# Performance work log

Measured on AMD Instinct MI355X. Metric: run time of the kernel, lower is better.

## Reference

```python
import jax, jax.numpy as jnp
import numpy as np

N = 50000      # nodes
E = 800000     # directed edges (self-loops added in reference)
F_IN = 64      # input features
HID = 64       # hidden channels
HEADS = 4
NCLS = 3
G = 64         # graphs in batch
EPS = 1e-5
NEG_SLOPE = 0.2


def setup_inputs() -> dict:
    key = jax.random.key(0)
    ks = jax.random.split(key, 20)
    s = 0.1
    inp = {
        "x": jax.random.normal(ks[0], (N, F_IN), jnp.float32),
        "edge_index": jax.random.randint(ks[1], (2, E), 0, N, jnp.int64),
        "batch": jnp.sort(jax.random.randint(ks[2], (N,), 0, G, jnp.int64)),
        # GATConv 1: F_IN -> HID per head, HEADS heads, concat
        "W1": jax.random.normal(ks[3], (F_IN, HEADS * HID), jnp.float32) * s,
        "a_src1": jax.random.normal(ks[4], (HEADS, HID), jnp.float32) * s,
        "a_dst1": jax.random.normal(ks[5], (HEADS, HID), jnp.float32) * s,
        "b1": jnp.zeros((HEADS * HID,), jnp.float32),
        # BatchNorm1d(256) eval-mode params
        "g1": jnp.ones((HEADS * HID,), jnp.float32),
        "be1": jnp.zeros((HEADS * HID,), jnp.float32),
        "m1": jnp.zeros((HEADS * HID,), jnp.float32),
        "v1": jnp.ones((HEADS * HID,), jnp.float32),
        # GATConv 2: 256 -> HID, 1 head
        "W2": jax.random.normal(ks[6], (HEADS * HID, HID), jnp.float32) * s,
        "a_src2": jax.random.normal(ks[7], (1, HID), jnp.float32) * s,
        "a_dst2": jax.random.normal(ks[8], (1, HID), jnp.float32) * s,
        "b2": jnp.zeros((HID,), jnp.float32),
        # BatchNorm1d(64)
        "g2": jnp.ones((HID,), jnp.float32),
        "be2": jnp.zeros((HID,), jnp.float32),
        "m2": jnp.zeros((HID,), jnp.float32),
        "v2": jnp.ones((HID,), jnp.float32),
        # MLP head
        "lw1": jax.random.normal(ks[9], (HID, HID // 2), jnp.float32) * s,
        "lb1": jnp.zeros((HID // 2,), jnp.float32),
        "lw2": jax.random.normal(ks[10], (HID // 2, NCLS), jnp.float32) * s,
        "lb2": jnp.zeros((NCLS,), jnp.float32),
    }
    return inp


def _gat(x, src, dst, W, a_s, a_d, b):
    """PyG-style GATConv: gather, LeakyReLU score, segment-softmax over dst, scatter-add."""
    H_, C_ = a_s.shape
    h = (x @ W).reshape(-1, H_, C_)                       # [N,H,C]
    es = jnp.einsum('nhc,hc->nh', h, a_s)                 # per-node src score
    ed = jnp.einsum('nhc,hc->nh', h, a_d)                 # per-node dst score
    e = jax.nn.leaky_relu(es[src] + ed[dst], NEG_SLOPE)   # [Etot,H]
    m = jax.ops.segment_max(e, dst, num_segments=N)       # stable softmax per dst
    p = jnp.exp(e - m[dst])
    denom = jax.ops.segment_sum(p, dst, num_segments=N)
    alpha = p / denom[dst]                                # [Etot,H]
    out = jax.ops.segment_sum(h[src] * alpha[:, :, None], dst, num_segments=N)
    return out.reshape(-1, H_ * C_) + b


def _bn(x, g, b, mean, var):
    return (x - mean) * jax.lax.rsqrt(var + EPS) * g + b


def reference(x, W1, a_src1, a_dst1, b1, g1, be1, m1, v1,
              W2, a_src2, a_dst2, b2, g2, be2, m2, v2,
              lw1, lb1, lw2, lb2, edge_index, batch):
    loop = jnp.arange(N, dtype=edge_index.dtype)
    src = jnp.concatenate([edge_index[0], loop])          # add self-loops
    dst = jnp.concatenate([edge_index[1], loop])
    h = _gat(x, src, dst, W1, a_src1, a_dst1, b1)
    h = jax.nn.elu(_bn(h, g1, be1, m1, v1))
    h = _gat(h, src, dst, W2, a_src2, a_dst2, b2)
    h = _bn(h, g2, be2, m2, v2)
    # global_mean_pool over graphs
    sums = jax.ops.segment_sum(h, batch, num_segments=G)
    cnt = jax.ops.segment_sum(jnp.ones((N, 1), h.dtype), batch, num_segments=G)
    pooled = sums / jnp.maximum(cnt, 1.0)                 # [G, HID]
    z = jax.nn.relu(pooled @ lw1 + lb1)
    z = z @ lw2 + lb2
    return jax.nn.log_softmax(z, axis=1)
```

## Files before the change

### kernel.cpp

```cpp
#include <hip/hip_runtime.h>
#include <math.h>

#define N_NODES 50000
#define N_EDGES 800000
#define ETOT    (N_EDGES + N_NODES)
#define GGRAPHS 64
#define EPS_BN  1e-5f

typedef __attribute__((ext_vector_type(8))) short short8;
typedef __attribute__((ext_vector_type(4))) float f32x4;
typedef __attribute__((ext_vector_type(2))) float f32x2;

__device__ __forceinline__ unsigned short f2bf(float f) {
    union { float f; unsigned u; } v; v.f = f;
    unsigned r = v.u + 0x7fffu + ((v.u >> 16) & 1u);
    return (unsigned short)(r >> 16);
}
__device__ __forceinline__ float leaky(float e) {
    return fmaxf(e, 0.2f * e);
}
__device__ __forceinline__ unsigned pack4_fp8(float a, float b, float c, float d) {
    int v = __builtin_amdgcn_cvt_pk_fp8_f32(a, b, 0, false);
    v = __builtin_amdgcn_cvt_pk_fp8_f32(c, d, v, true);
    return (unsigned)v;
}
__device__ __forceinline__ short8 cvt8(const float* p) {
    float4 u = *(const float4*)p;
    float4 v = *(const float4*)(p + 4);
    short8 r;
    r[0] = (short)f2bf(u.x); r[1] = (short)f2bf(u.y);
    r[2] = (short)f2bf(u.z); r[3] = (short)f2bf(u.w);
    r[4] = (short)f2bf(v.x); r[5] = (short)f2bf(v.y);
    r[6] = (short)f2bf(v.z); r[7] = (short)f2bf(v.w);
    return r;
}

#define NBUK 196
#define EPB  4096
#define NBLK2 ((ETOT + EPB - 1) / EPB)
#define CAP  8192


#define PREP2_T (32768 + 320)

__global__ void k_prep(const float* __restrict__ W1, const float* __restrict__ W2,
                       const float* __restrict__ b1, const float* __restrict__ g1,
                       const float* __restrict__ be1, const float* __restrict__ m1,
                       const float* __restrict__ v1,
                       const float* __restrict__ b2, const float* __restrict__ g2,
                       const float* __restrict__ be2, const float* __restrict__ m2,
                       const float* __restrict__ v2,
                       unsigned short* __restrict__ W1T,
                       unsigned short* __restrict__ W2T,
                       float* __restrict__ A1s, float* __restrict__ B1s,
                       float* __restrict__ A2s, float* __restrict__ B2s) {
    int t = blockIdx.x * 256 + threadIdx.x;
    if (t < 16384) {
        int i = t;
        int n = i >> 6, k = i & 63;
        W1T[i] = f2bf(W1[k * 256 + n]);
    } else if (t < 32768) {
        int i = t - 16384;
        int n = i >> 8, kp = i & 255;
        int rk = (kp & 15) * 16 + (kp >> 4);
        W2T[i] = f2bf(W2[rk * 64 + n]);
    } else if (t < 32768 + 256) {
        int z = t - 32768;
        int r = (z & 15) * 16 + (z >> 4);
        float A = g1[r] * rsqrtf(v1[r] + EPS_BN);
        A1s[z] = A;
        B1s[z] = (b1[r] - m1[r]) * A + be1[r];
    } else if (t < PREP2_T) {
        int z = t - 32768 - 256;
        int r = (z & 3) * 16 + (z >> 2);
        float A = g2[r] * rsqrtf(v2[r] + EPS_BN);
        A2s[z] = A;
        B2s[z] = (b2[r] - m2[r]) * A + be2[r];
    }
}


__global__ __launch_bounds__(256)
void k_bhist(const int* __restrict__ ei, int* __restrict__ gcnt) {
    __shared__ int c[NBUK];
    int t = threadIdx.x;
    for (int i = t; i < NBUK; i += 256) c[i] = 0;
    __syncthreads();
    int e0 = blockIdx.x * EPB;
#pragma unroll
    for (int j = 0; j < EPB / 256; ++j) {
        int e = e0 + j * 256 + t;
        if (e < ETOT) {
            int d = (e < N_EDGES) ? ei[N_EDGES + e] : (e - N_EDGES);
            atomicAdd(&c[d >> 8], 1);
        }
    }
    __syncthreads();
    for (int i = t; i < NBUK; i += 256) gcnt[i * NBLK2 + blockIdx.x] = c[i];
}

__global__ __launch_bounds__(256)
void k_bsum(const int* __restrict__ gcnt, int* __restrict__ bstart,
            int* __restrict__ offs) {
    __shared__ int s[256];
    int t = threadIdx.x;
    int total = 0;
    if (t < NBUK)
        for (int b = 0; b < NBLK2; ++b) total += gcnt[t * NBLK2 + b];
    s[t] = total; __syncthreads();
    for (int d2 = 1; d2 < 256; d2 <<= 1) {
        int add = (t >= d2) ? s[t - d2] : 0;
        __syncthreads();
        s[t] += add;
        __syncthreads();
    }
    if (t < NBUK) bstart[t] = s[t] - total;
    if (t == 0) { bstart[NBUK] = ETOT; offs[N_NODES] = ETOT; }
}

__global__ __launch_bounds__(256)
void k_bscan(const int* __restrict__ gcnt, const int* __restrict__ bstart,
             int* __restrict__ gbase) {
    __shared__ int s[256];
    int b = blockIdx.x, t = threadIdx.x;
    int v = (t < NBLK2) ? gcnt[b * NBLK2 + t] : 0;
    s[t] = v; __syncthreads();
    for (int d2 = 1; d2 < 256; d2 <<= 1) {
        int add = (t >= d2) ? s[t - d2] : 0;
        __syncthreads();
        s[t] += add;
        __syncthreads();
    }
    int base = bstart[b];
    if (t < NBLK2) gbase[b * NBLK2 + t] = base + s[t] - v;
}

__global__ __launch_bounds__(256)
void k_bfill(const int* __restrict__ ei, const int* __restrict__ gbase,
             unsigned* __restrict__ pairs) {
    __shared__ int cur[NBUK];
    int t = threadIdx.x;
    for (int i = t; i < NBUK; i += 256) cur[i] = gbase[i * NBLK2 + blockIdx.x];
    __syncthreads();
    int e0 = blockIdx.x * EPB;
#pragma unroll
    for (int j = 0; j < EPB / 256; ++j) {
        int e = e0 + j * 256 + t;
        if (e < ETOT) {
            int s, d;
            if (e < N_EDGES) { s = ei[e]; d = ei[N_EDGES + e]; }
            else             { s = d = e - N_EDGES; }
            int pos = atomicAdd(&cur[d >> 8], 1);
            pairs[pos] = (unsigned)s | ((unsigned)d << 16);
        }
    }
}

__global__ __launch_bounds__(256)
void k_csr(const unsigned* __restrict__ pairs, const int* __restrict__ bstart,
           int* __restrict__ offs, unsigned short* __restrict__ csr) {
    __shared__ unsigned sp[CAP];
    __shared__ unsigned short lc[CAP];
    __shared__ int c256[256];
    __shared__ int o256[256];
    __shared__ int s[256];
    int b = blockIdx.x, t = threadIdx.x;
    int base = bstart[b];
    int n = bstart[b + 1] - base;
    int node = b * 256 + t;
    if (n <= CAP) {
        for (int i = t; i < n; i += 256) sp[i] = pairs[base + i];
        c256[t] = 0;
        __syncthreads();
        for (int i = t; i < n; i += 256) atomicAdd(&c256[(sp[i] >> 16) & 255], 1);
        __syncthreads();
        int v = c256[t];
        s[t] = v; __syncthreads();
        for (int d2 = 1; d2 < 256; d2 <<= 1) {
            int add = (t >= d2) ? s[t - d2] : 0;
            __syncthreads();
            s[t] += add;
            __syncthreads();
        }
        int myoff = s[t] - v;
        o256[t] = myoff;
        if (node < N_NODES) offs[node] = base + myoff;
        __syncthreads();
        for (int i = t; i < n; i += 256) {
            unsigned p = sp[i];
            int pos = atomicAdd(&o256[(p >> 16) & 255], 1);
            lc[pos] = (unsigned short)(p & 0xffff);
        }
        __syncthreads();
        for (int i = t; i < n; i += 256) csr[base + i] = lc[i];
    } else {
        c256[t] = 0;
        __syncthreads();
        for (int i = t; i < n; i += 256) atomicAdd(&c256[(pairs[base + i] >> 16) & 255], 1);
        __syncthreads();
        int v = c256[t];
        s[t] = v; __syncthreads();
        for (int d2 = 1; d2 < 256; d2 <<= 1) {
            int add = (t >= d2) ? s[t - d2] : 0;
            __syncthreads();
            s[t] += add;
            __syncthreads();
        }
        int myoff = s[t] - v;
        o256[t] = base + myoff;
        if (node < N_NODES) offs[node] = base + myoff;
        __syncthreads();
        for (int i = t; i < n; i += 256) {
            unsigned p = pairs[base + i];
            int pos = atomicAdd(&o256[(p >> 16) & 255], 1);
            csr[pos] = (unsigned short)(p & 0xffff);
        }
    }
}


__global__ __launch_bounds__(256)
void k_gemm1(const float* __restrict__ x, const unsigned short* __restrict__ W1Tg,
             const float* __restrict__ a_s, const float* __restrict__ a_d,
             unsigned char* __restrict__ h1f8, float* __restrict__ es1, float* __restrict__ ed1) {
    __shared__ unsigned short W1T[256 * 72];
    int t = threadIdx.x;
    for (int c = t; c < 2048; c += 256) {
        int n = c >> 3, k8 = (c & 7) * 8;
        *(short8*)&W1T[n * 72 + k8] = *(const short8*)&W1Tg[n * 64 + k8];
    }
    __syncthreads();
    int wid = t >> 6, lane = t & 63;
    int quad = lane >> 4, col = lane & 15;
    float as_r[16], ad_r[16];
#pragma unroll
    for (int i = 0; i < 16; ++i) {
        as_r[i] = a_s[i * 16 + col];
        ad_r[i] = a_d[i * 16 + col];
    }
    int tile = blockIdx.x * 4 + wid;
    if (tile >= 3125) return;
    int base = tile * 16;
    short8 a0 = cvt8(&x[(size_t)(base + col) * 64 + quad * 8]);
    short8 a1 = cvt8(&x[(size_t)(base + col) * 64 + 32 + quad * 8]);
    f32x4 acc[16];
#pragma unroll
    for (int nt = 0; nt < 16; ++nt) acc[nt] = (f32x4){0.f, 0.f, 0.f, 0.f};
#pragma unroll
    for (int nt = 0; nt < 16; ++nt) {
        short8 b0 = *(const short8*)&W1T[(nt * 16 + col) * 72 + quad * 8];
        short8 b1 = *(const short8*)&W1T[(nt * 16 + col) * 72 + 32 + quad * 8];
        acc[nt] = __builtin_amdgcn_mfma_f32_16x16x32_bf16(a0, b0, acc[nt], 0, 0, 0);
        acc[nt] = __builtin_amdgcn_mfma_f32_16x16x32_bf16(a1, b1, acc[nt], 0, 0, 0);
    }
    float esp[16], edp[16];
#pragma unroll
    for (int i = 0; i < 16; ++i) { esp[i] = 0.f; edp[i] = 0.f; }
#pragma unroll
    for (int nt = 0; nt < 16; ++nt) {
        int hd = nt >> 2;
#pragma unroll
        for (int r = 0; r < 4; ++r) {
            esp[hd * 4 + r] += acc[nt][r] * as_r[nt];
            edp[hd * 4 + r] += acc[nt][r] * ad_r[nt];
        }
    }
#pragma unroll
    for (int i = 0; i < 16; ++i) {
        float v = esp[i], w = edp[i];
#pragma unroll
        for (int m = 1; m <= 8; m <<= 1) { v += __shfl_xor(v, m); w += __shfl_xor(w, m); }
        esp[i] = v; edp[i] = w;
    }
    if (col == 0) {
#pragma unroll
        for (int hd = 0; hd < 4; ++hd)
#pragma unroll
            for (int r = 0; r < 4; ++r) {
                int node = base + quad * 4 + r;
                es1[node * 4 + hd] = esp[hd * 4 + r];
                ed1[node * 4 + hd] = edp[hd * 4 + r];
            }
    }
#pragma unroll
    for (int r = 0; r < 4; ++r) {
        uint4 pk;
        pk.x = pack4_fp8(acc[0][r],  acc[1][r],  acc[2][r],  acc[3][r]);
        pk.y = pack4_fp8(acc[4][r],  acc[5][r],  acc[6][r],  acc[7][r]);
        pk.z = pack4_fp8(acc[8][r],  acc[9][r],  acc[10][r], acc[11][r]);
        pk.w = pack4_fp8(acc[12][r], acc[13][r], acc[14][r], acc[15][r]);
        *(uint4*)&h1f8[(size_t)(base + quad * 4 + r) * 256 + col * 16] = pk;
    }
}


__global__ __launch_bounds__(256)
void k_gat1(const unsigned char* __restrict__ h1f8, const float* __restrict__ es1,
            const float* __restrict__ ed1, const int* __restrict__ offs,
            const unsigned short* __restrict__ csr,
            const float* __restrict__ A1s, const float* __restrict__ B1s,
            unsigned short* __restrict__ hb) {
    int tid = threadIdx.x;
    int l = tid & 63;
    int gbase = l & 48;
    int q = tid & 15;
    int d = blockIdx.x * 16 + (tid >> 4);
    int start = offs[d], deg = offs[d + 1] - start;
    int e4 = q >> 2, hd = q & 3;
    float edv = ed1[d * 4 + hd];
    const unsigned char* hrow = h1f8 + q * 16;
    float a[16];
#pragma unroll
    for (int i = 0; i < 16; ++i) a[i] = 0.f;
    float wsum = 0.f;
    for (int c0 = 0; c0 < deg; c0 += 4) {
        int idx = c0 + e4;
        int s = csr[start + min(idx, deg - 1)];
        float w = (idx < deg) ? __expf(leaky(es1[s * 4 + hd] + edv)) : 0.f;
        wsum += w;
        int se[4];
#pragma unroll
        for (int e = 0; e < 4; ++e) se[e] = __shfl(s, gbase | (e << 2));
        uint4 rv[4];
#pragma unroll
        for (int e = 0; e < 4; ++e)
            rv[e] = *(const uint4*)(hrow + ((size_t)(unsigned)se[e] << 8));
#pragma unroll
        for (int e = 0; e < 4; ++e) {
            float w0 = __shfl(w, gbase | (e << 2) | 0);
            float w1 = __shfl(w, gbase | (e << 2) | 1);
            float w2 = __shfl(w, gbase | (e << 2) | 2);
            float w3 = __shfl(w, gbase | (e << 2) | 3);
            f32x2 p;
            p = __builtin_amdgcn_cvt_pk_f32_fp8((int)rv[e].x, false); a[0]  += w0 * p.x; a[1]  += w0 * p.y;
            p = __builtin_amdgcn_cvt_pk_f32_fp8((int)rv[e].x, true);  a[2]  += w0 * p.x; a[3]  += w0 * p.y;
            p = __builtin_amdgcn_cvt_pk_f32_fp8((int)rv[e].y, false); a[4]  += w1 * p.x; a[5]  += w1 * p.y;
            p = __builtin_amdgcn_cvt_pk_f32_fp8((int)rv[e].y, true);  a[6]  += w1 * p.x; a[7]  += w1 * p.y;
            p = __builtin_amdgcn_cvt_pk_f32_fp8((int)rv[e].z, false); a[8]  += w2 * p.x; a[9]  += w2 * p.y;
            p = __builtin_amdgcn_cvt_pk_f32_fp8((int)rv[e].z, true);  a[10] += w2 * p.x; a[11] += w2 * p.y;
            p = __builtin_amdgcn_cvt_pk_f32_fp8((int)rv[e].w, false); a[12] += w3 * p.x; a[13] += w3 * p.y;
            p = __builtin_amdgcn_cvt_pk_f32_fp8((int)rv[e].w, true);  a[14] += w3 * p.x; a[15] += w3 * p.y;
        }
    }
    wsum += __shfl_xor(wsum, 4);
    wsum += __shfl_xor(wsum, 8);
    float inv[4];
#pragma unroll
    for (int h = 0; h < 4; ++h) inv[h] = 1.f / __shfl(wsum, gbase | h);
    ushort4 ov[4];
#pragma unroll
    for (int i0 = 0; i0 < 4; ++i0) {
        float4 Av = *(const float4*)&A1s[q * 16 + i0 * 4];
        float4 Bv = *(const float4*)&B1s[q * 16 + i0 * 4];
        float o0 = a[i0 * 4 + 0] * inv[i0] * Av.x + Bv.x;
        float o1 = a[i0 * 4 + 1] * inv[i0] * Av.y + Bv.y;
        float o2 = a[i0 * 4 + 2] * inv[i0] * Av.z + Bv.z;
        float o3 = a[i0 * 4 + 3] * inv[i0] * Av.w + Bv.w;
        o0 = (o0 > 0.f) ? o0 : expm1f(o0);
        o1 = (o1 > 0.f) ? o1 : expm1f(o1);
        o2 = (o2 > 0.f) ? o2 : expm1f(o2);
        o3 = (o3 > 0.f) ? o3 : expm1f(o3);
        ov[i0].x = f2bf(o0); ov[i0].y = f2bf(o1); ov[i0].z = f2bf(o2); ov[i0].w = f2bf(o3);
    }
#pragma unroll
    for (int i0 = 0; i0 < 4; ++i0)
        *(ushort4*)&hb[(size_t)d * 256 + q * 16 + i0 * 4] = ov[i0];
}


__global__ __launch_bounds__(256)
void k_gemm2(const unsigned short* __restrict__ hbbf, const unsigned short* __restrict__ W2Tg,
             const float* __restrict__ a_s, const float* __restrict__ a_d,
             unsigned char* __restrict__ h2f8, float* __restrict__ es2, float* __restrict__ ed2) {
    __shared__ unsigned short W2T[64 * 264];
    int t = threadIdx.x;
    for (int c = t; c < 2048; c += 256) {
        int n = c >> 5, k8 = (c & 31) * 8;
        *(short8*)&W2T[n * 264 + k8] = *(const short8*)&W2Tg[n * 256 + k8];
    }
    __syncthreads();
    int wid = t >> 6, lane = t & 63;
    int quad = lane >> 4, col = lane & 15;
    float as_r[4], ad_r[4];
#pragma unroll
    for (int i = 0; i < 4; ++i) {
        as_r[i] = a_s[i * 16 + col];
        ad_r[i] = a_d[i * 16 + col];
    }
    int tile = blockIdx.x * 4 + wid;
    if (tile >= 3125) return;
    int base = tile * 16;
    short8 af[8];
#pragma unroll
    for (int kk = 0; kk < 8; ++kk)
        af[kk] = *(const short8*)&hbbf[(size_t)(base + col) * 256 + kk * 32 + quad * 8];
    f32x4 acc[4];
#pragma unroll
    for (int nt = 0; nt < 4; ++nt) acc[nt] = (f32x4){0.f, 0.f, 0.f, 0.f};
#pragma unroll
    for (int kk = 0; kk < 8; ++kk) {
#pragma unroll
        for (int nt = 0; nt < 4; ++nt) {
            short8 b = *(const short8*)&W2T[(nt * 16 + col) * 264 + kk * 32 + quad * 8];
            acc[nt] = __builtin_amdgcn_mfma_f32_16x16x32_bf16(af[kk], b, acc[nt], 0, 0, 0);
        }
    }
    float esp[4], edp[4];
#pragma unroll
    for (int r = 0; r < 4; ++r) { esp[r] = 0.f; edp[r] = 0.f; }
#pragma unroll
    for (int nt = 0; nt < 4; ++nt)
#pragma unroll
        for (int r = 0; r < 4; ++r) {
            esp[r] += acc[nt][r] * as_r[nt];
            edp[r] += acc[nt][r] * ad_r[nt];
        }
#pragma unroll
    for (int r = 0; r < 4; ++r) {
        float v = esp[r], w = edp[r];
#pragma unroll
        for (int m = 1; m <= 8; m <<= 1) { v += __shfl_xor(v, m); w += __shfl_xor(w, m); }
        esp[r] = v; edp[r] = w;
    }
    if (col == 0) {
#pragma unroll
        for (int r = 0; r < 4; ++r) {
            int node = base + quad * 4 + r;
            es2[node] = esp[r];
            ed2[node] = edp[r];
        }
    }
#pragma unroll
    for (int r = 0; r < 4; ++r) {
        unsigned pk = pack4_fp8(acc[0][r], acc[1][r], acc[2][r], acc[3][r]);
        *(unsigned*)&h2f8[(size_t)(base + quad * 4 + r) * 64 + col * 4] = pk;
    }
}


__global__ __launch_bounds__(256)
void k_gat2(const unsigned char* __restrict__ h2f8, const float* __restrict__ es2,
            const float* __restrict__ ed2, const int* __restrict__ offs,
            const unsigned short* __restrict__ csr,
            const float* __restrict__ A2s, const float* __restrict__ B2s,
            float* __restrict__ out2) {
    int tid = threadIdx.x;
    int l = tid & 63;
    int gbase = l & 48;
    int q = tid & 15;
    int d = blockIdx.x * 16 + (tid >> 4);
    int start = offs[d], deg = offs[d + 1] - start;
    float edv = ed2[d];
    const unsigned char* hrow = h2f8 + q * 4;
    float a0 = 0.f, a1 = 0.f, a2 = 0.f, a3 = 0.f, wsum = 0.f;
    int e4 = q & 3;
    for (int c0 = 0; c0 < deg; c0 += 4) {
        int idx = c0 + e4;
        int s = csr[start + min(idx, deg - 1)];
        float w = (idx < deg) ? __expf(leaky(es2[s] + edv)) : 0.f;
        wsum += w;
        int se[4];
#pragma unroll
        for (int e = 0; e < 4; ++e) se[e] = __shfl(s, gbase | e);
        unsigned rv[4];
#pragma unroll
        for (int e = 0; e < 4; ++e)
            rv[e] = *(const unsigned*)(hrow + ((size_t)(unsigned)se[e] << 6));
#pragma unroll
        for (int e = 0; e < 4; ++e) {
            float we = __shfl(w, gbase | e);
            f32x2 p;
            p = __builtin_amdgcn_cvt_pk_f32_fp8((int)rv[e], false); a0 += we * p.x; a1 += we * p.y;
            p = __builtin_amdgcn_cvt_pk_f32_fp8((int)rv[e], true);  a2 += we * p.x; a3 += we * p.y;
        }
    }
    wsum += __shfl_xor(wsum, 1);
    wsum += __shfl_xor(wsum, 2);
    float inv = 1.f / wsum;
    float4 Av = *(const float4*)&A2s[q * 4];
    float4 Bv = *(const float4*)&B2s[q * 4];
    float4 o;
    o.x = a0 * inv * Av.x + Bv.x;
    o.y = a1 * inv * Av.y + Bv.y;
    o.z = a2 * inv * Av.z + Bv.z;
    o.w = a3 * inv * Av.w + Bv.w;
    *(float4*)&out2[(size_t)d * 64 + q * 4] = o;
}


#define POOLB ((N_NODES + 127) / 128)

__global__ __launch_bounds__(256)
void k_pool1(const float* __restrict__ out2, const int* __restrict__ batch,
             float* __restrict__ pooled) {
    int t = threadIdx.x;
    int sub = t >> 6, ch = t & 63;
    int istart = blockIdx.x * 128 + sub * 32;
    int iend = min(istart + 32, N_NODES);
    if (istart >= N_NODES) return;
    int curg = batch[istart];
    float acc = 0.f;
    for (int i = istart; i < iend; ++i) {
        int g = batch[i];
        if (g != curg) {
            atomicAdd(&pooled[curg * 64 + ch], acc);
            acc = 0.f;
            curg = g;
        }
        acc += out2[(size_t)i * 64 + ch];
    }
    atomicAdd(&pooled[curg * 64 + ch], acc);
}


__device__ int lower_bound_i(const int* a, int n, int key) {
    int lo = 0, hi = n;
    while (lo < hi) {
        int mid = (lo + hi) >> 1;
        if (a[mid] < key) lo = mid + 1; else hi = mid;
    }
    return lo;
}

__global__ void k_head(const float* __restrict__ pooled, const int* __restrict__ batch,
                       const float* __restrict__ lw1, const float* __restrict__ lb1,
                       const float* __restrict__ lw2, const float* __restrict__ lb2,
                       float* __restrict__ out) {
    int g = threadIdx.x;
    if (g >= GGRAPHS) return;
    int s0 = lower_bound_i(batch, N_NODES, g);
    int s1 = lower_bound_i(batch, N_NODES, g + 1);
    int cnt = s1 - s0;
    float invc = 1.f / (float)((cnt > 0) ? cnt : 1);
    float p[64];
#pragma unroll
    for (int c = 0; c < 64; ++c) p[c] = pooled[g * 64 + c] * invc;
    float z0 = lb2[0], z1 = lb2[1], z2 = lb2[2];
    for (int j = 0; j < 32; ++j) {
        float hj = lb1[j];
#pragma unroll
        for (int c = 0; c < 64; ++c) {
            int rc = (c & 3) * 16 + (c >> 2);
            hj += p[c] * lw1[rc * 32 + j];
        }
        hj = fmaxf(hj, 0.f);
        z0 += hj * lw2[j * 3 + 0];
        z1 += hj * lw2[j * 3 + 1];
        z2 += hj * lw2[j * 3 + 2];
    }
    float m = fmaxf(z0, fmaxf(z1, z2));
    float lse = logf(expf(z0 - m) + expf(z1 - m) + expf(z2 - m)) + m;
    out[g * 3 + 0] = z0 - lse;
    out[g * 3 + 1] = z1 - lse;
    out[g * 3 + 2] = z2 - lse;
}


extern "C" void kernel_launch(void* const* d_in, const int* in_sizes, int n_in,
                              void* d_out, int out_size, void* d_ws, size_t ws_size,
                              hipStream_t stream) {
    (void)in_sizes; (void)n_in; (void)out_size; (void)ws_size;
    const float* x    = (const float*)d_in[0];
    const int*   ei   = (const int*)d_in[1];
    const int*   batch= (const int*)d_in[2];
    const float* W1   = (const float*)d_in[3];
    const float* a_s1 = (const float*)d_in[4];
    const float* a_d1 = (const float*)d_in[5];
    const float* b1   = (const float*)d_in[6];
    const float* g1   = (const float*)d_in[7];
    const float* be1  = (const float*)d_in[8];
    const float* m1   = (const float*)d_in[9];
    const float* v1   = (const float*)d_in[10];
    const float* W2   = (const float*)d_in[11];
    const float* a_s2 = (const float*)d_in[12];
    const float* a_d2 = (const float*)d_in[13];
    const float* b2   = (const float*)d_in[14];
    const float* g2   = (const float*)d_in[15];
    const float* be2  = (const float*)d_in[16];
    const float* m2   = (const float*)d_in[17];
    const float* v2   = (const float*)d_in[18];
    const float* lw1  = (const float*)d_in[19];
    const float* lb1  = (const float*)d_in[20];
    const float* lw2  = (const float*)d_in[21];
    const float* lb2  = (const float*)d_in[22];
    float* out = (float*)d_out;

    char* ws = (char*)d_ws;
    size_t off = 0;
    auto alloc = [&](size_t bytes) -> void* {
        void* p = ws + off;
        off += (bytes + 255) & ~(size_t)255;
        return p;
    };
    unsigned short* W1T = (unsigned short*)alloc((size_t)16384 * 2);
    unsigned short* W2T = (unsigned short*)alloc((size_t)16384 * 2);
    unsigned char*  h1  = (unsigned char*)alloc((size_t)N_NODES * 256);
    unsigned short* hb  = (unsigned short*)alloc((size_t)N_NODES * 256 * 2);
    unsigned char*  h2  = (unsigned char*)alloc((size_t)N_NODES * 64);
    float* out2 = (float*)alloc((size_t)N_NODES * 64 * 4);
    float* es1  = (float*)alloc((size_t)N_NODES * 4 * 4);
    float* ed1  = (float*)alloc((size_t)N_NODES * 4 * 4);
    float* es2  = (float*)alloc((size_t)N_NODES * 4);
    float* ed2  = (float*)alloc((size_t)N_NODES * 4);
    float* pooled = (float*)alloc((size_t)GGRAPHS * 64 * 4);
    float* A1s  = (float*)alloc(256 * 4);
    float* B1s  = (float*)alloc(256 * 4);
    float* A2s  = (float*)alloc(64 * 4);
    float* B2s  = (float*)alloc(64 * 4);
    int*   offs = (int*)alloc((size_t)(N_NODES + 1) * 4);
    unsigned short* csr = (unsigned short*)alloc((size_t)ETOT * 2);
    unsigned* pairs = (unsigned*)alloc((size_t)ETOT * 4);
    int* gcnt  = (int*)alloc((size_t)NBUK * NBLK2 * 4);
    int* gbase = (int*)alloc((size_t)NBUK * NBLK2 * 4);
    int* bstart = (int*)alloc((size_t)(NBUK + 1) * 4);

    const int ntileb = (3125 + 3) / 4;
    const int ngat = 3125;
    const int nprep = (PREP2_T + 255) / 256;

    hipMemsetAsync(pooled, 0, (size_t)GGRAPHS * 64 * 4, stream);
    k_prep<<<nprep, 256, 0, stream>>>(W1, W2, b1, g1, be1, m1, v1,
                                      b2, g2, be2, m2, v2,
                                      W1T, W2T, A1s, B1s, A2s, B2s);
    k_bhist<<<NBLK2, 256, 0, stream>>>(ei, gcnt);
    k_bsum<<<1, 256, 0, stream>>>(gcnt, bstart, offs);
    k_bscan<<<NBUK, 256, 0, stream>>>(gcnt, bstart, gbase);
    k_bfill<<<NBLK2, 256, 0, stream>>>(ei, gbase, pairs);
    k_csr<<<NBUK, 256, 0, stream>>>(pairs, bstart, offs, csr);

    k_gemm1<<<ntileb, 256, 0, stream>>>(x, W1T, a_s1, a_d1, h1, es1, ed1);
    k_gat1<<<ngat, 256, 0, stream>>>(h1, es1, ed1, offs, csr, A1s, B1s, hb);
    k_gemm2<<<ntileb, 256, 0, stream>>>(hb, W2T, a_s2, a_d2, h2, es2, ed2);
    k_gat2<<<ngat, 256, 0, stream>>>(h2, es2, ed2, offs, csr, A2s, B2s, out2);
    k_pool1<<<POOLB, 256, 0, stream>>>(out2, batch, pooled);
    k_head<<<1, 64, 0, stream>>>(pooled, batch, lw1, lb1, lw2, lb2, out);
}
```

Baseline: 259.7 us.

## Fuse CSR build passes, fuse GAT1 with GEMM2 and GAT2 with pooling

Replaces the histogram/scan/fill CSR pipeline with a single pass that appends edges into fixed-capacity per-bucket regions using a global atomic cursor, and merges weight prep into the same launch. Fuses the layer-1 aggregation with the second projection GEMM via shared memory, avoiding the bf16 intermediate in global memory. Fuses the layer-2 aggregation with mean pooling so the fp32 node output is never stored. Adds a risk of silently dropping edges if a bucket exceeds its fixed capacity, and uses less reused W2 in the fused GEMM.

```diff
diff --git a/kernel.cpp b/kernel.cpp
--- a/kernel.cpp
+++ b/kernel.cpp
@@ -38,92 +38,95 @@
 #define NBUK 196
 #define EPB  4096
 #define NBLK2 ((ETOT + EPB - 1) / EPB)
-#define CAP  8192
+#define CAPR 6144
 
 
 #define PREP2_T (32768 + 320)
-
-__global__ void k_prep(const float* __restrict__ W1, const float* __restrict__ W2,
-                       const float* __restrict__ b1, const float* __restrict__ g1,
-                       const float* __restrict__ be1, const float* __restrict__ m1,
-                       const float* __restrict__ v1,
-                       const float* __restrict__ b2, const float* __restrict__ g2,
-                       const float* __restrict__ be2, const float* __restrict__ m2,
-                       const float* __restrict__ v2,
-                       unsigned short* __restrict__ W1T,
-                       unsigned short* __restrict__ W2T,
-                       float* __restrict__ A1s, float* __restrict__ B1s,
-                       float* __restrict__ A2s, float* __restrict__ B2s) {
-    int t = blockIdx.x * 256 + threadIdx.x;
-    if (t < 16384) {
-        int i = t;
-        int n = i >> 6, k = i & 63;
-        W1T[i] = f2bf(W1[k * 256 + n]);
-    } else if (t < 32768) {
-        int i = t - 16384;
-        int n = i >> 8, kp = i & 255;
-        int rk = (kp & 15) * 16 + (kp >> 4);
-        W2T[i] = f2bf(W2[rk * 64 + n]);
-    } else if (t < 32768 + 256) {
-        int z = t - 32768;
-        int r = (z & 15) * 16 + (z >> 4);
-        float A = g1[r] * rsqrtf(v1[r] + EPS_BN);
-        A1s[z] = A;
-        B1s[z] = (b1[r] - m1[r]) * A + be1[r];
-    } else if (t < PREP2_T) {
-        int z = t - 32768 - 256;
-        int r = (z & 3) * 16 + (z >> 2);
-        float A = g2[r] * rsqrtf(v2[r] + EPS_BN);
-        A2s[z] = A;
-        B2s[z] = (b2[r] - m2[r]) * A + be2[r];
-    }
-}
-
+#define NPREP ((PREP2_T + 255) / 256)
 
 __global__ __launch_bounds__(256)
-void k_bhist(const int* __restrict__ ei, int* __restrict__ gcnt) {
-    __shared__ int c[NBUK];
+void k_prepfill(const float* __restrict__ W1, const float* __restrict__ W2,
+                const float* __restrict__ b1, const float* __restrict__ g1,
+                const float* __restrict__ be1, const float* __restrict__ m1,
+                const float* __restrict__ v1,
+                const float* __restrict__ b2, const float* __restrict__ g2,
+                const float* __restrict__ be2, const float* __restrict__ m2,
+                const float* __restrict__ v2,
+                const int* __restrict__ ei,
+                unsigned short* __restrict__ W1T,
+                unsigned short* __restrict__ W2T,
+                float* __restrict__ A1s, float* __restrict__ B1s,
+                float* __restrict__ A2s, float* __restrict__ B2s,
+                int* __restrict__ gcur, unsigned* __restrict__ pairs) {
+    __shared__ int lcnt[NBUK];
+    __shared__ int lbase[NBUK];
+    if (blockIdx.x < NPREP) {
+        int t = blockIdx.x * 256 + threadIdx.x;
+        if (t < 16384) {
+            int i = t;
+            int n = i >> 6, k = i & 63;
+            W1T[i] = f2bf(W1[k * 256 + n]);
+        } else if (t < 32768) {
+            int i = t - 16384;
+            int n = i >> 8, kp = i & 255;
+            int rk = (kp & 15) * 16 + (kp >> 4);
+            W2T[i] = f2bf(W2[rk * 64 + n]);
+        } else if (t < 32768 + 256) {
+            int z = t - 32768;
+            int r = (z & 15) * 16 + (z >> 4);
+            float A = g1[r] * rsqrtf(v1[r] + EPS_BN);
+            A1s[z] = A;
+            B1s[z] = (b1[r] - m1[r]) * A + be1[r];
+        } else if (t < PREP2_T) {
+            int z = t - 32768 - 256;
+            int r = (z & 3) * 16 + (z >> 2);
+            float A = g2[r] * rsqrtf(v2[r] + EPS_BN);
+            A2s[z] = A;
+            B2s[z] = (b2[r] - m2[r]) * A + be2[r];
+        }
+        return;
+    }
     int t = threadIdx.x;
-    for (int i = t; i < NBUK; i += 256) c[i] = 0;
-    __syncthreads();
-    int e0 = blockIdx.x * EPB;
-#pragma unroll
-    for (int j = 0; j < EPB / 256; ++j) {
+    int blk = blockIdx.x - NPREP;
+    for (int i = t; i < NBUK; i += 256) lcnt[i] = 0;
+    __syncthreads();
+    int e0 = blk * EPB;
+    int ds[16], ss[16];
+#pragma unroll
+    for (int j = 0; j < 16; ++j) {
         int e = e0 + j * 256 + t;
+        int s = -1, d = -1;
         if (e < ETOT) {
-            int d = (e < N_EDGES) ? ei[N_EDGES + e] : (e - N_EDGES);
-            atomicAdd(&c[d >> 8], 1);
-        }
-    }
-    __syncthreads();
-    for (int i = t; i < NBUK; i += 256) gcnt[i * NBLK2 + blockIdx.x] = c[i];
-}
+            if (e < N_EDGES) { s = ei[e]; d = ei[N_EDGES + e]; }
+            else             { s = d = e - N_EDGES; }
+            atomicAdd(&lcnt[d >> 8], 1);
+        }
+        ds[j] = d; ss[j] = s;
+    }
+    __syncthreads();
+    for (int i = t; i < NBUK; i += 256) {
+        int c = lcnt[i];
+        lbase[i] = i * CAPR + (c ? atomicAdd(&gcur[i], c) : 0);
+    }
+    __syncthreads();
+#pragma unroll
+    for (int j = 0; j < 16; ++j) {
+        if (ds[j] >= 0) {
+            int bk = ds[j] >> 8;
+            int pos = atomicAdd(&lbase[bk], 1);
+            if (pos < (bk + 1) * CAPR)
+                pairs[pos] = (unsigned)ss[j] | ((unsigned)(ds[j] & 255) << 16);
+        }
+    }
+}
+
 
 __global__ __launch_bounds__(256)
-void k_bsum(const int* __restrict__ gcnt, int* __restrict__ bstart,
+void k_bsum(const int* __restrict__ gcur, int* __restrict__ bstart,
             int* __restrict__ offs) {
     __shared__ int s[256];
     int t = threadIdx.x;
-    int total = 0;
-    if (t < NBUK)
-        for (int b = 0; b < NBLK2; ++b) total += gcnt[t * NBLK2 + b];
-    s[t] = total; __syncthreads();
-    for (int d2 = 1; d2 < 256; d2 <<= 1) {
-        int add = (t >= d2) ? s[t - d2] : 0;
-        __syncthreads();
-        s[t] += add;
-        __syncthreads();
-    }
-    if (t < NBUK) bstart[t] = s[t] - total;
-    if (t == 0) { bstart[NBUK] = ETOT; offs[N_NODES] = ETOT; }
-}
-
-__global__ __launch_bounds__(256)
-void k_bscan(const int* __restrict__ gcnt, const int* __restrict__ bstart,
-             int* __restrict__ gbase) {
-    __shared__ int s[256];
-    int b = blockIdx.x, t = threadIdx.x;
-    int v = (t < NBLK2) ? gcnt[b * NBLK2 + t] : 0;
+    int v = (t < NBUK) ? gcur[t] : 0;
     s[t] = v; __syncthreads();
     for (int d2 = 1; d2 < 256; d2 <<= 1) {
         int add = (t >= d2) ? s[t - d2] : 0;
@@ -131,34 +134,17 @@
         s[t] += add;
         __syncthreads();
     }
-    int base = bstart[b];
-    if (t < NBLK2) gbase[b * NBLK2 + t] = base + s[t] - v;
-}
+    if (t < NBUK) bstart[t] = s[t] - v;
+    if (t == 0) { bstart[NBUK] = ETOT; offs[N_NODES] = ETOT; }
+}
+
+
+#define CAP 6144
 
 __global__ __launch_bounds__(256)
-void k_bfill(const int* __restrict__ ei, const int* __restrict__ gbase,
-             unsigned* __restrict__ pairs) {
-    __shared__ int cur[NBUK];
-    int t = threadIdx.x;
-    for (int i = t; i < NBUK; i += 256) cur[i] = gbase[i * NBLK2 + blockIdx.x];
-    __syncthreads();
-    int e0 = blockIdx.x * EPB;
-#pragma unroll
-    for (int j = 0; j < EPB / 256; ++j) {
-        int e = e0 + j * 256 + t;
-        if (e < ETOT) {
-            int s, d;
-            if (e < N_EDGES) { s = ei[e]; d = ei[N_EDGES + e]; }
-            else             { s = d = e - N_EDGES; }
-            int pos = atomicAdd(&cur[d >> 8], 1);
-            pairs[pos] = (unsigned)s | ((unsigned)d << 16);
-        }
-    }
-}
-
-__global__ __launch_bounds__(256)
-void k_csr(const unsigned* __restrict__ pairs, const int* __restrict__ bstart,
-           int* __restrict__ offs, unsigned short* __restrict__ csr) {
+void k_csr(const unsigned* __restrict__ pairs, const int* __restrict__ gcur,
+           const int* __restrict__ bstart, int* __restrict__ offs,
+           unsigned short* __restrict__ csr) {
     __shared__ unsigned sp[CAP];
     __shared__ unsigned short lc[CAP];
     __shared__ int c256[256];
@@ -166,56 +152,33 @@
     __shared__ int s[256];
     int b = blockIdx.x, t = threadIdx.x;
     int base = bstart[b];
-    int n = bstart[b + 1] - base;
+    int n = gcur[b];
     int node = b * 256 + t;
-    if (n <= CAP) {
-        for (int i = t; i < n; i += 256) sp[i] = pairs[base + i];
-        c256[t] = 0;
+    const unsigned* reg = pairs + (size_t)b * CAPR;
+    for (int i = t; i < n; i += 256) sp[i] = reg[i];
+    c256[t] = 0;
+    __syncthreads();
+    for (int i = t; i < n; i += 256) atomicAdd(&c256[(sp[i] >> 16) & 255], 1);
+    __syncthreads();
+    int v = c256[t];
+    s[t] = v; __syncthreads();
+    for (int d2 = 1; d2 < 256; d2 <<= 1) {
+        int add = (t >= d2) ? s[t - d2] : 0;
         __syncthreads();
-        for (int i = t; i < n; i += 256) atomicAdd(&c256[(sp[i] >> 16) & 255], 1);
+        s[t] += add;
         __syncthreads();
-        int v = c256[t];
-        s[t] = v; __syncthreads();
-        for (int d2 = 1; d2 < 256; d2 <<= 1) {
-            int add = (t >= d2) ? s[t - d2] : 0;
-            __syncthreads();
-            s[t] += add;
-            __syncthreads();
-        }
-        int myoff = s[t] - v;
-        o256[t] = myoff;
-        if (node < N_NODES) offs[node] = base + myoff;
-        __syncthreads();
-        for (int i = t; i < n; i += 256) {
-            unsigned p = sp[i];
-            int pos = atomicAdd(&o256[(p >> 16) & 255], 1);
-            lc[pos] = (unsigned short)(p & 0xffff);
-        }
-        __syncthreads();
-        for (int i = t; i < n; i += 256) csr[base + i] = lc[i];
-    } else {
-        c256[t] = 0;
-        __syncthreads();
-        for (int i = t; i < n; i += 256) atomicAdd(&c256[(pairs[base + i] >> 16) & 255], 1);
-        __syncthreads();
-        int v = c256[t];
-        s[t] = v; __syncthreads();
-        for (int d2 = 1; d2 < 256; d2 <<= 1) {
-            int add = (t >= d2) ? s[t - d2] : 0;
-            __syncthreads();
-            s[t] += add;
-            __syncthreads();
-        }
-        int myoff = s[t] - v;
-        o256[t] = base + myoff;
-        if (node < N_NODES) offs[node] = base + myoff;
-        __syncthreads();
-        for (int i = t; i < n; i += 256) {
-            unsigned p = pairs[base + i];
-            int pos = atomicAdd(&o256[(p >> 16) & 255], 1);
-            csr[pos] = (unsigned short)(p & 0xffff);
-        }
-    }
+    }
+    int myoff = s[t] - v;
+    o256[t] = myoff;
+    if (node < N_NODES) offs[node] = base + myoff;
+    __syncthreads();
+    for (int i = t; i < n; i += 256) {
+        unsigned p = sp[i];
+        int pos = atomicAdd(&o256[(p >> 16) & 255], 1);
+        lc[pos] = (unsigned short)(p & 0xffff);
+    }
+    __syncthreads();
+    for (int i = t; i < n; i += 256) csr[base + i] = lc[i];
 }
 
 
@@ -295,16 +258,25 @@
 
 
 __global__ __launch_bounds__(256)
-void k_gat1(const unsigned char* __restrict__ h1f8, const float* __restrict__ es1,
-            const float* __restrict__ ed1, const int* __restrict__ offs,
-            const unsigned short* __restrict__ csr,
-            const float* __restrict__ A1s, const float* __restrict__ B1s,
-            unsigned short* __restrict__ hb) {
+void k_gat1g2(const unsigned char* __restrict__ h1f8, const float* __restrict__ es1,
+              const float* __restrict__ ed1, const int* __restrict__ offs,
+              const unsigned short* __restrict__ csr,
+              const float* __restrict__ A1s, const float* __restrict__ B1s,
+              const unsigned short* __restrict__ W2Tg,
+              const float* __restrict__ a_s2, const float* __restrict__ a_d2,
+              unsigned char* __restrict__ h2f8, float* __restrict__ es2,
+              float* __restrict__ ed2) {
+    __shared__ unsigned short hbt[16][264];
+    __shared__ float esps[4][16], edps[4][16];
+    __shared__ uint4 h2t4[64];
+    unsigned char* h2t = (unsigned char*)h2t4;
     int tid = threadIdx.x;
     int l = tid & 63;
     int gbase = l & 48;
     int q = tid & 15;
-    int d = blockIdx.x * 16 + (tid >> 4);
+    int dl = tid >> 4;
+    int nbase = blockIdx.x * 16;
+    int d = nbase + dl;
     int start = offs[d], deg = offs[d + 1] - start;
     int e4 = q >> 2, hd = q & 3;
     float edv = ed1[d * 4 + hd];
@@ -347,7 +319,6 @@
     float inv[4];
 #pragma unroll
     for (int h = 0; h < 4; ++h) inv[h] = 1.f / __shfl(wsum, gbase | h);
-    ushort4 ov[4];
 #pragma unroll
     for (int i0 = 0; i0 < 4; ++i0) {
         float4 Av = *(const float4*)&A1s[q * 16 + i0 * 4];
@@ -360,95 +331,74 @@
         o1 = (o1 > 0.f) ? o1 : expm1f(o1);
         o2 = (o2 > 0.f) ? o2 : expm1f(o2);
         o3 = (o3 > 0.f) ? o3 : expm1f(o3);
-        ov[i0].x = f2bf(o0); ov[i0].y = f2bf(o1); ov[i0].z = f2bf(o2); ov[i0].w = f2bf(o3);
-    }
-#pragma unroll
-    for (int i0 = 0; i0 < 4; ++i0)
-        *(ushort4*)&hb[(size_t)d * 256 + q * 16 + i0 * 4] = ov[i0];
+        ushort4 ov;
+        ov.x = f2bf(o0); ov.y = f2bf(o1); ov.z = f2bf(o2); ov.w = f2bf(o3);
+        *(ushort4*)&hbt[dl][q * 16 + i0 * 4] = ov;
+    }
+    __syncthreads();
+    int w = tid >> 6;
+    int quad = l >> 4, col = l & 15;
+    short8 af[8];
+#pragma unroll
+    for (int kk = 0; kk < 8; ++kk)
+        af[kk] = *(const short8*)&hbt[col][kk * 32 + quad * 8];
+    f32x4 acc = (f32x4){0.f, 0.f, 0.f, 0.f};
+#pragma unroll
+    for (int kk = 0; kk < 8; ++kk) {
+        short8 b = *(const short8*)&W2Tg[(w * 16 + col) * 256 + kk * 32 + quad * 8];
+        acc = __builtin_amdgcn_mfma_f32_16x16x32_bf16(af[kk], b, acc, 0, 0, 0);
+    }
+    float asw = a_s2[w * 16 + col], adw = a_d2[w * 16 + col];
+    float esp[4], edp[4];
+#pragma unroll
+    for (int r = 0; r < 4; ++r) { esp[r] = acc[r] * asw; edp[r] = acc[r] * adw; }
+#pragma unroll
+    for (int r = 0; r < 4; ++r) {
+#pragma unroll
+        for (int m = 1; m <= 8; m <<= 1) {
+            esp[r] += __shfl_xor(esp[r], m);
+            edp[r] += __shfl_xor(edp[r], m);
+        }
+    }
+    if (col == 0) {
+#pragma unroll
+        for (int r = 0; r < 4; ++r) {
+            esps[w][quad * 4 + r] = esp[r];
+            edps[w][quad * 4 + r] = edp[r];
+        }
+    }
+#pragma unroll
+    for (int r = 0; r < 4; ++r) {
+        unsigned pk = pack4_fp8(acc[r], acc[r], acc[r], acc[r]);
+        h2t[(quad * 4 + r) * 64 + col * 4 + w] = (unsigned char)(pk & 0xff);
+    }
+    __syncthreads();
+    if (tid < 16) {
+        es2[nbase + tid] = esps[0][tid] + esps[1][tid] + esps[2][tid] + esps[3][tid];
+        ed2[nbase + tid] = edps[0][tid] + edps[1][tid] + edps[2][tid] + edps[3][tid];
+    }
+    if (tid < 64) {
+        int node = tid >> 2, c = tid & 3;
+        *(uint4*)&h2f8[(size_t)(nbase + node) * 64 + c * 16] = h2t4[node * 4 + c];
+    }
 }
 
 
 __global__ __launch_bounds__(256)
-void k_gemm2(const unsigned short* __restrict__ hbbf, const unsigned short* __restrict__ W2Tg,
-             const float* __restrict__ a_s, const float* __restrict__ a_d,
-             unsigned char* __restrict__ h2f8, float* __restrict__ es2, float* __restrict__ ed2) {
-    __shared__ unsigned short W2T[64 * 264];
-    int t = threadIdx.x;
-    for (int c = t; c < 2048; c += 256) {
-        int n = c >> 5, k8 = (c & 31) * 8;
-        *(short8*)&W2T[n * 264 + k8] = *(const short8*)&W2Tg[n * 256 + k8];
-    }
-    __syncthreads();
-    int wid = t >> 6, lane = t & 63;
-    int quad = lane >> 4, col = lane & 15;
-    float as_r[4], ad_r[4];
-#pragma unroll
-    for (int i = 0; i < 4; ++i) {
-        as_r[i] = a_s[i * 16 + col];
-        ad_r[i] = a_d[i * 16 + col];
-    }
-    int tile = blockIdx.x * 4 + wid;
-    if (tile >= 3125) return;
-    int base = tile * 16;
-    short8 af[8];
-#pragma unroll
-    for (int kk = 0; kk < 8; ++kk)
-        af[kk] = *(const short8*)&hbbf[(size_t)(base + col) * 256 + kk * 32 + quad * 8];
-    f32x4 acc[4];
-#pragma unroll
-    for (int nt = 0; nt < 4; ++nt) acc[nt] = (f32x4){0.f, 0.f, 0.f, 0.f};
-#pragma unroll
-    for (int kk = 0; kk < 8; ++kk) {
-#pragma unroll
-        for (int nt = 0; nt < 4; ++nt) {
-            short8 b = *(const short8*)&W2T[(nt * 16 + col) * 264 + kk * 32 + quad * 8];
-            acc[nt] = __builtin_amdgcn_mfma_f32_16x16x32_bf16(af[kk], b, acc[nt], 0, 0, 0);
-        }
-    }
-    float esp[4], edp[4];
-#pragma unroll
-    for (int r = 0; r < 4; ++r) { esp[r] = 0.f; edp[r] = 0.f; }
-#pragma unroll
-    for (int nt = 0; nt < 4; ++nt)
-#pragma unroll
-        for (int r = 0; r < 4; ++r) {
-            esp[r] += acc[nt][r] * as_r[nt];
-            edp[r] += acc[nt][r] * ad_r[nt];
-        }
-#pragma unroll
-    for (int r = 0; r < 4; ++r) {
-        float v = esp[r], w = edp[r];
-#pragma unroll
-        for (int m = 1; m <= 8; m <<= 1) { v += __shfl_xor(v, m); w += __shfl_xor(w, m); }
-        esp[r] = v; edp[r] = w;
-    }
-    if (col == 0) {
-#pragma unroll
-        for (int r = 0; r < 4; ++r) {
-            int node = base + quad * 4 + r;
-            es2[node] = esp[r];
-            ed2[node] = edp[r];
-        }
-    }
-#pragma unroll
-    for (int r = 0; r < 4; ++r) {
-        unsigned pk = pack4_fp8(acc[0][r], acc[1][r], acc[2][r], acc[3][r]);
-        *(unsigned*)&h2f8[(size_t)(base + quad * 4 + r) * 64 + col * 4] = pk;
-    }
-}
-
-
-__global__ __launch_bounds__(256)
-void k_gat2(const unsigned char* __restrict__ h2f8, const float* __restrict__ es2,
-            const float* __restrict__ ed2, const int* __restrict__ offs,
-            const unsigned short* __restrict__ csr,
-            const float* __restrict__ A2s, const float* __restrict__ B2s,
-            float* __restrict__ out2) {
+void k_gat2p(const unsigned char* __restrict__ h2f8, const float* __restrict__ es2,
+             const float* __restrict__ ed2, const int* __restrict__ offs,
+             const unsigned short* __restrict__ csr,
+             const float* __restrict__ A2s, const float* __restrict__ B2s,
+             const int* __restrict__ batch, float* __restrict__ pooled) {
+    __shared__ float ot[16][68];
+    __shared__ int gbat[16];
     int tid = threadIdx.x;
     int l = tid & 63;
     int gbase = l & 48;
     int q = tid & 15;
-    int d = blockIdx.x * 16 + (tid >> 4);
+    int dl = tid >> 4;
+    int nbase = blockIdx.x * 16;
+    int d = nbase + dl;
     int start = offs[d], deg = offs[d + 1] - start;
     float edv = ed2[d];
     const unsigned char* hrow = h2f8 + q * 4;
@@ -479,37 +429,28 @@
     float inv = 1.f / wsum;
     float4 Av = *(const float4*)&A2s[q * 4];
     float4 Bv = *(const float4*)&B2s[q * 4];
-    float4 o;
-    o.x = a0 * inv * Av.x + Bv.x;
-    o.y = a1 * inv * Av.y + Bv.y;
-    o.z = a2 * inv * Av.z + Bv.z;
-    o.w = a3 * inv * Av.w + Bv.w;
-    *(float4*)&out2[(size_t)d * 64 + q * 4] = o;
-}
-
-
-#define POOLB ((N_NODES + 127) / 128)
-
-__global__ __launch_bounds__(256)
-void k_pool1(const float* __restrict__ out2, const int* __restrict__ batch,
-             float* __restrict__ pooled) {
-    int t = threadIdx.x;
-    int sub = t >> 6, ch = t & 63;
-    int istart = blockIdx.x * 128 + sub * 32;
-    int iend = min(istart + 32, N_NODES);
-    if (istart >= N_NODES) return;
-    int curg = batch[istart];
-    float acc = 0.f;
-    for (int i = istart; i < iend; ++i) {
-        int g = batch[i];
-        if (g != curg) {
-            atomicAdd(&pooled[curg * 64 + ch], acc);
-            acc = 0.f;
-            curg = g;
-        }
-        acc += out2[(size_t)i * 64 + ch];
-    }
-    atomicAdd(&pooled[curg * 64 + ch], acc);
+    ot[dl][q * 4 + 0] = a0 * inv * Av.x + Bv.x;
+    ot[dl][q * 4 + 1] = a1 * inv * Av.y + Bv.y;
+    ot[dl][q * 4 + 2] = a2 * inv * Av.z + Bv.z;
+    ot[dl][q * 4 + 3] = a3 * inv * Av.w + Bv.w;
+    if (tid < 16) gbat[tid] = batch[nbase + tid];
+    __syncthreads();
+    if (tid < 64) {
+        int ch = tid;
+        int curg = gbat[0];
+        float acc = 0.f;
+#pragma unroll
+        for (int n = 0; n < 16; ++n) {
+            int g = gbat[n];
+            if (g != curg) {
+                atomicAdd(&pooled[curg * 64 + ch], acc);
+                acc = 0.f;
+                curg = g;
+            }
+            acc += ot[n][ch];
+        }
+        atomicAdd(&pooled[curg * 64 + ch], acc);
+    }
 }
 
 
@@ -592,46 +533,40 @@
         off += (bytes + 255) & ~(size_t)255;
         return p;
     };
+    float* pooled = (float*)alloc((size_t)GGRAPHS * 64 * 4);
+    int*   gcur   = (int*)alloc((size_t)NBUK * 4);
     unsigned short* W1T = (unsigned short*)alloc((size_t)16384 * 2);
     unsigned short* W2T = (unsigned short*)alloc((size_t)16384 * 2);
     unsigned char*  h1  = (unsigned char*)alloc((size_t)N_NODES * 256);
-    unsigned short* hb  = (unsigned short*)alloc((size_t)N_NODES * 256 * 2);
     unsigned char*  h2  = (unsigned char*)alloc((size_t)N_NODES * 64);
-    float* out2 = (float*)alloc((size_t)N_NODES * 64 * 4);
     float* es1  = (float*)alloc((size_t)N_NODES * 4 * 4);
     float* ed1  = (float*)alloc((size_t)N_NODES * 4 * 4);
     float* es2  = (float*)alloc((size_t)N_NODES * 4);
     float* ed2  = (float*)alloc((size_t)N_NODES * 4);
-    float* pooled = (float*)alloc((size_t)GGRAPHS * 64 * 4);
     float* A1s  = (float*)alloc(256 * 4);
     float* B1s  = (float*)alloc(256 * 4);
     float* A2s  = (float*)alloc(64 * 4);
     float* B2s  = (float*)alloc(64 * 4);
     int*   offs = (int*)alloc((size_t)(N_NODES + 1) * 4);
     unsigned short* csr = (unsigned short*)alloc((size_t)ETOT * 2);
-    unsigned* pairs = (unsigned*)alloc((size_t)ETOT * 4);
-    int* gcnt  = (int*)alloc((size_t)NBUK * NBLK2 * 4);
-    int* gbase = (int*)alloc((size_t)NBUK * NBLK2 * 4);
+    unsigned* pairs = (unsigned*)alloc((size_t)NBUK * CAPR * 4);
     int* bstart = (int*)alloc((size_t)(NBUK + 1) * 4);
 
     const int ntileb = (3125 + 3) / 4;
     const int ngat = 3125;
-    const int nprep = (PREP2_T + 255) / 256;
-
-    hipMemsetAsync(pooled, 0, (size_t)GGRAPHS * 64 * 4, stream);
-    k_prep<<<nprep, 256, 0, stream>>>(W1, W2, b1, g1, be1, m1, v1,
-                                      b2, g2, be2, m2, v2,
-                                      W1T, W2T, A1s, B1s, A2s, B2s);
-    k_bhist<<<NBLK2, 256, 0, stream>>>(ei, gcnt);
-    k_bsum<<<1, 256, 0, stream>>>(gcnt, bstart, offs);
-    k_bscan<<<NBUK, 256, 0, stream>>>(gcnt, bstart, gbase);
-    k_bfill<<<NBLK2, 256, 0, stream>>>(ei, gbase, pairs);
-    k_csr<<<NBUK, 256, 0, stream>>>(pairs, bstart, offs, csr);
+
+    hipMemsetAsync(pooled, 0, 16384 + 1024, stream);
+    k_prepfill<<<NPREP + NBLK2, 256, 0, stream>>>(W1, W2, b1, g1, be1, m1, v1,
+                                                  b2, g2, be2, m2, v2, ei,
+                                                  W1T, W2T, A1s, B1s, A2s, B2s,
+                                                  gcur, pairs);
+    k_bsum<<<1, 256, 0, stream>>>(gcur, bstart, offs);
+    k_csr<<<NBUK, 256, 0, stream>>>(pairs, gcur, bstart, offs, csr);
 
     k_gemm1<<<ntileb, 256, 0, stream>>>(x, W1T, a_s1, a_d1, h1, es1, ed1);
-    k_gat1<<<ngat, 256, 0, stream>>>(h1, es1, ed1, offs, csr, A1s, B1s, hb);
-    k_gemm2<<<ntileb, 256, 0, stream>>>(hb, W2T, a_s2, a_d2, h2, es2, ed2);
-    k_gat2<<<ngat, 256, 0, stream>>>(h2, es2, ed2, offs, csr, A2s, B2s, out2);
-    k_pool1<<<POOLB, 256, 0, stream>>>(out2, batch, pooled);
+    k_gat1g2<<<ngat, 256, 0, stream>>>(h1, es1, ed1, offs, csr, A1s, B1s,
+                                       W2T, a_s2, a_d2, h2, es2, ed2);
+    k_gat2p<<<ngat, 256, 0, stream>>>(h2, es2, ed2, offs, csr, A2s, B2s,
+                                      batch, pooled);
     k_head<<<1, 64, 0, stream>>>(pooled, batch, lw1, lb1, lw2, lb2, out);
 }
```

Measured after the change: 236.4 us. 9.0% less time.
